# Performance work log

Measured on AMD Instinct MI355X. Metric: run time of the kernel, lower is better.

Reference implementation:

```python
import jax, jax.numpy as jnp
import numpy as np

HM_W, WH_W, OFF_W = 1.0, 0.1, 1.0  # loss_weight dict values
EPS_SIG = 1e-4


def _neg_loss(pred, gt):
    # pred already sigmoided + clamped. Modified focal loss (CornerNet).
    pos = (gt == 1.0).astype(pred.dtype)
    neg = (gt < 1.0).astype(pred.dtype)
    part1 = (pos + (2.0 * neg - 1.0) * pred) ** 2          # alpha=2
    part2 = (neg + (2.0 * pos - 1.0) * gt) ** 4            # beta=4
    part3 = jnp.log(neg + (2.0 * pos - 1.0) * pred)
    loss = -jnp.sum(part1 * part2 * part3)
    num_pos = jnp.sum(pos)
    fallback = jnp.maximum(jnp.sum((pred > 0.3).astype(pred.dtype)), 1.0)
    denom = jnp.where(num_pos == 0.0, fallback, num_pos)
    return loss / denom


def _reg_l1(pred, mask, ind, target):
    # pred: [B,C,H,W] -> gather K per-object C-dim vectors per batch via flat HW index
    B, C, H, W = pred.shape
    K = ind.shape[1]
    feat = pred.transpose(0, 2, 3, 1).reshape(B, H * W, C)  # [B,HW,C]
    idx = jnp.broadcast_to(ind[:, :, None], (B, K, C))
    gathered = jnp.take_along_axis(feat, idx, axis=1)       # [B,K,C]
    m = jnp.broadcast_to(mask[:, :, None].astype(pred.dtype), (B, K, C))
    diff = gathered * m - target * m
    ad = jnp.abs(diff)
    sl1 = jnp.where(ad < 1.0, 0.5 * diff * diff, ad - 0.5)  # smooth_l1, sum
    return jnp.sum(sl1) / (jnp.sum(m) + 1e-4)


def setup_inputs() -> dict:
    key = jax.random.key(0)
    ks = jax.random.split(key, 8)
    B, C, H, W, K = 128, 20, 128, 128, 128
    hm_pred = jax.random.normal(ks[0], (B, C, H, W), dtype=jnp.float32)
    hm_gt = jax.random.uniform(ks[1], (B, C, H, W), dtype=jnp.float32)
    # plant some exact positives (gt == 1) like real CenterNet targets
    hm_gt = hm_gt.at[:, :, 64, 64].set(1.0)
    wh_pred = jax.random.normal(ks[2], (B, 2, H, W), dtype=jnp.float32)
    wh_gt = jax.random.uniform(ks[3], (B, K, 2), dtype=jnp.float32)
    off_pred = jax.random.normal(ks[4], (B, 2, H, W), dtype=jnp.float32)
    off_gt = jax.random.uniform(ks[5], (B, K, 2), dtype=jnp.float32)
    offset_mask = jax.random.randint(ks[6], (B, K), 0, 2, dtype=jnp.int32)
    indexes = jax.random.randint(ks[7], (B, K), 0, H * W).astype(jnp.int64)
    return {"hm_pred": hm_pred, "hm_gt": hm_gt, "wh_pred": wh_pred,
            "wh_gt": wh_gt, "off_pred": off_pred, "off_gt": off_gt,
            "offset_mask": offset_mask, "indexes": indexes}


def reference(hm_pred, hm_gt, wh_pred, wh_gt, off_pred, off_gt, offset_mask, indexes):
    hm = jnp.clip(jax.nn.sigmoid(hm_pred), EPS_SIG, 1.0 - EPS_SIG)
    hm_loss = _neg_loss(hm, hm_gt)
    wh_loss = _reg_l1(wh_pred, offset_mask, indexes, wh_gt)
    off_loss = _reg_l1(off_pred, offset_mask, indexes, off_gt)
    total = HM_W * hm_loss + WH_W * wh_loss + OFF_W * off_loss
    return (hm_loss, wh_loss, off_loss, total)
```

## Files before the change

kernel.cpp:

```cpp
#include <hip/hip_runtime.h>

#define NB_HM   2048
#define NB_REG  64
#define REG_OFF (3 * NB_HM)

typedef float f32x4 __attribute__((ext_vector_type(4)));

__device__ __forceinline__ float wave_sum(float v) {
    #pragma unroll
    for (int off = 32; off > 0; off >>= 1) v += __shfl_down(v, off, 64);
    return v;
}

__device__ __forceinline__ void block_reduce_store3(float a, float b, float c,
                                                    float* __restrict__ dst) {
    a = wave_sum(a); b = wave_sum(b); c = wave_sum(c);
    __shared__ float sa[8], sb[8], sc[8];
    int lane = threadIdx.x & 63;
    int wave = threadIdx.x >> 6;
    if (lane == 0) { sa[wave] = a; sb[wave] = b; sc[wave] = c; }
    __syncthreads();
    if (threadIdx.x == 0) {
        int nw = blockDim.x >> 6;
        float ta = 0.f, tb = 0.f, tc = 0.f;
        for (int w = 0; w < nw; ++w) { ta += sa[w]; tb += sb[w]; tc += sc[w]; }
        dst[0] = ta; dst[1] = tb; dst[2] = tc;
    }
}

__device__ __forceinline__ void hm_elem(float x, float gt, float& s_loss,
                                        unsigned& posc, unsigned& cntc) {
    bool pos = (gt == 1.0f);
    float e = __expf(-x);
    float p = __builtin_amdgcn_rcpf(1.0f + e);
    p = fminf(fmaxf(p, 1e-4f), 1.0f - 1e-4f);
    float arg = pos ? p : 1.0f - p;
    float a   = 1.0f - arg;
    float b   = pos ? 1.0f : 1.0f - gt;
    float b2  = b * b;
    float l   = __logf(arg);
    s_loss += (a * a) * (b2 * b2) * l;
    posc += (unsigned)__popcll(__ballot(pos));
    cntc += (unsigned)__popcll(__ballot(p > 0.3f));
}

#define COMPV(P, G)                                    \
    do {                                               \
        hm_elem((P)[0], (G)[0], s_loss, posc, cntc);   \
        hm_elem((P)[1], (G)[1], s_loss, posc, cntc);   \
        hm_elem((P)[2], (G)[2], s_loss, posc, cntc);   \
        hm_elem((P)[3], (G)[3], s_loss, posc, cntc);   \
    } while (0)

__global__ void __launch_bounds__(256)
hm_loss_kernel(const f32x4* __restrict__ p4,
               const f32x4* __restrict__ g4,
               float* __restrict__ ws, long long N4) {
    float    s_loss = 0.f;
    unsigned posc = 0, cntc = 0;

    if ((N4 % ((long long)NB_HM * 256)) == 0) {
        long long per_block = N4 / NB_HM;
        long long nIter     = per_block >> 8;
        long long i = (long long)blockIdx.x * per_block + threadIdx.x;

        long long j = 0;
        for (; j + 3 < nIter; j += 4, i += 1024) {
            f32x4 xp0 = p4[i];
            f32x4 xp1 = p4[i + 256];
            f32x4 xp2 = p4[i + 512];
            f32x4 xp3 = p4[i + 768];
            f32x4 xg0 = g4[i];
            f32x4 xg1 = g4[i + 256];
            f32x4 xg2 = g4[i + 512];
            f32x4 xg3 = g4[i + 768];
            COMPV(xp0, xg0);
            COMPV(xp1, xg1);
            COMPV(xp2, xg2);
            COMPV(xp3, xg3);
        }
        for (; j < nIter; ++j, i += 256) {
            f32x4 xp = p4[i];
            f32x4 xg = g4[i];
            COMPV(xp, xg);
        }
    } else {
        long long tid = (long long)blockIdx.x * blockDim.x + threadIdx.x;
        long long NT  = (long long)gridDim.x * blockDim.x;
        for (long long i = tid; i < N4; i += NT) {
            f32x4 xp = p4[i];
            f32x4 xg = g4[i];
            COMPV(xp, xg);
        }
    }

    int lane = threadIdx.x & 63;
    float fpos = (lane == 0) ? (float)posc : 0.f;
    float fcnt = (lane == 0) ? (float)cntc : 0.f;
    block_reduce_store3(s_loss, fpos, fcnt, &ws[3 * (size_t)blockIdx.x]);
}

__device__ __forceinline__ float smooth_l1(float d) {
    float ad = fabsf(d);
    return (ad < 1.0f) ? 0.5f * d * d : ad - 0.5f;
}

__global__ void __launch_bounds__(256)
reg_loss_kernel(const float* __restrict__ wh_pred,  const float* __restrict__ wh_gt,
                const float* __restrict__ off_pred, const float* __restrict__ off_gt,
                const int* __restrict__ mask, const int* __restrict__ ind,
                float* __restrict__ ws, int BK, int K, int HW) {
    int t = blockIdx.x * blockDim.x + threadIdx.x;
    int nt = gridDim.x * blockDim.x;
    float s_wh = 0.f, s_off = 0.f, s_m = 0.f;

    for (int i = t; i < BK; i += nt) {
        int b   = i / K;
        float m = (float)mask[i];
        int idx = ind[i];
        const float* wb = wh_pred  + (size_t)b * 2 * HW;
        const float* ob = off_pred + (size_t)b * 2 * HW;
        #pragma unroll
        for (int c = 0; c < 2; ++c) {
            float gw = wb[(size_t)c * HW + idx];
            float tw = wh_gt[(size_t)i * 2 + c];
            s_wh += smooth_l1(gw * m - tw * m);

            float go = ob[(size_t)c * HW + idx];
            float to = off_gt[(size_t)i * 2 + c];
            s_off += smooth_l1(go * m - to * m);
        }
        s_m += 2.0f * m;
    }

    block_reduce_store3(s_wh, s_off, s_m, &ws[REG_OFF + 3 * (size_t)blockIdx.x]);
}

__global__ void __launch_bounds__(1024)
reduce_finalize_kernel(const float* __restrict__ ws, float* __restrict__ out) {
    float a = 0.f, b = 0.f, c = 0.f, w = 0.f, o = 0.f, m = 0.f;
    for (int i = threadIdx.x; i < NB_HM; i += 1024) {
        a += ws[3 * i + 0];
        b += ws[3 * i + 1];
        c += ws[3 * i + 2];
    }
    if (threadIdx.x < 3 * NB_REG) {
        float v = ws[REG_OFF + threadIdx.x];
        int r = threadIdx.x % 3;
        w = (r == 0) ? v : 0.f;
        o = (r == 1) ? v : 0.f;
        m = (r == 2) ? v : 0.f;
    }

    a = wave_sum(a); b = wave_sum(b); c = wave_sum(c);
    w = wave_sum(w); o = wave_sum(o); m = wave_sum(m);

    __shared__ float s[6][16];
    int lane = threadIdx.x & 63, wv = threadIdx.x >> 6;
    if (lane == 0) {
        s[0][wv] = a; s[1][wv] = b; s[2][wv] = c;
        s[3][wv] = w; s[4][wv] = o; s[5][wv] = m;
    }
    __syncthreads();
    if (threadIdx.x == 0) {
        float t[6];
        #pragma unroll
        for (int k = 0; k < 6; ++k) {
            float acc = 0.f;
            for (int q = 0; q < 16; ++q) acc += s[k][q];
            t[k] = acc;
        }
        float loss_sum = -t[0];
        float num_pos  = t[1];
        float fallback = fmaxf(t[2], 1.0f);
        float denom    = (num_pos == 0.0f) ? fallback : num_pos;
        float hm_loss  = loss_sum / denom;
        float md       = t[5] + 1e-4f;
        float wh_loss  = t[3] / md;
        float off_loss = t[4] / md;
        out[0] = hm_loss;
        out[1] = wh_loss;
        out[2] = off_loss;
        out[3] = hm_loss + 0.1f * wh_loss + off_loss;
    }
}

extern "C" void kernel_launch(void* const* d_in, const int* in_sizes, int n_in,
                              void* d_out, int out_size, void* d_ws, size_t ws_size,
                              hipStream_t stream) {
    const float* hm_pred  = (const float*)d_in[0];
    const float* hm_gt    = (const float*)d_in[1];
    const float* wh_pred  = (const float*)d_in[2];
    const float* wh_gt    = (const float*)d_in[3];
    const float* off_pred = (const float*)d_in[4];
    const float* off_gt   = (const float*)d_in[5];
    const int*   mask     = (const int*)d_in[6];
    const int*   ind      = (const int*)d_in[7];
    float*       out      = (float*)d_out;
    float*       ws       = (float*)d_ws;

    long long N  = in_sizes[0];
    int       BK = in_sizes[6];
    const int K  = 128;
    int       B  = BK / K;
    int       HW = in_sizes[2] / (2 * B);

    hm_loss_kernel<<<NB_HM, 256, 0, stream>>>((const f32x4*)hm_pred,
                                              (const f32x4*)hm_gt, ws, N >> 2);
    reg_loss_kernel<<<NB_REG, 256, 0, stream>>>(wh_pred, wh_gt, off_pred, off_gt,
                                                mask, ind, ws, BK, K, HW);
    reduce_finalize_kernel<<<1, 1024, 0, stream>>>(ws, out);
}
```

Baseline: 72.14 us.

## Fuse final reduction into regression kernel via last-block atomic counter; double hm blocks

Removes the separate single-block finalize kernel: the regression kernel's blocks increment an atomic counter, and the last block to finish reads all partial sums and writes the outputs. The counter is reset by the first block of the heatmap kernel, which runs earlier in the same stream. The heatmap grid is doubled to 4096 blocks, so each block handles less data and the final pass reduces more partials. This drops one kernel launch in exchange for a fence and an atomic per regression block.

```diff
diff --git a/kernel.cpp b/kernel.cpp
--- a/kernel.cpp
+++ b/kernel.cpp
@@ -1,8 +1,9 @@
 #include <hip/hip_runtime.h>
 
-#define NB_HM   2048
+#define NB_HM   4096
 #define NB_REG  64
 #define REG_OFF (3 * NB_HM)
+#define CTR_IDX (REG_OFF + 3 * NB_REG)
 
 typedef float f32x4 __attribute__((ext_vector_type(4)));
 
@@ -15,15 +16,15 @@
 __device__ __forceinline__ void block_reduce_store3(float a, float b, float c,
                                                     float* __restrict__ dst) {
     a = wave_sum(a); b = wave_sum(b); c = wave_sum(c);
-    __shared__ float sa[8], sb[8], sc[8];
+    __shared__ float sa[4], sb[4], sc[4];
     int lane = threadIdx.x & 63;
     int wave = threadIdx.x >> 6;
     if (lane == 0) { sa[wave] = a; sb[wave] = b; sc[wave] = c; }
     __syncthreads();
     if (threadIdx.x == 0) {
-        int nw = blockDim.x >> 6;
         float ta = 0.f, tb = 0.f, tc = 0.f;
-        for (int w = 0; w < nw; ++w) { ta += sa[w]; tb += sb[w]; tc += sc[w]; }
+        #pragma unroll
+        for (int w = 0; w < 4; ++w) { ta += sa[w]; tb += sb[w]; tc += sc[w]; }
         dst[0] = ta; dst[1] = tb; dst[2] = tc;
     }
 }
@@ -56,6 +57,9 @@
 hm_loss_kernel(const f32x4* __restrict__ p4,
                const f32x4* __restrict__ g4,
                float* __restrict__ ws, long long N4) {
+    if (blockIdx.x == 0 && threadIdx.x == 0)
+        *(volatile int*)&ws[CTR_IDX] = 0;
+
     float    s_loss = 0.f;
     unsigned posc = 0, cntc = 0;
 
@@ -106,12 +110,13 @@
 }
 
 __global__ void __launch_bounds__(256)
-reg_loss_kernel(const float* __restrict__ wh_pred,  const float* __restrict__ wh_gt,
-                const float* __restrict__ off_pred, const float* __restrict__ off_gt,
-                const int* __restrict__ mask, const int* __restrict__ ind,
-                float* __restrict__ ws, int BK, int K, int HW) {
-    int t = blockIdx.x * blockDim.x + threadIdx.x;
-    int nt = gridDim.x * blockDim.x;
+reg_finalize_kernel(const float* __restrict__ wh_pred,  const float* __restrict__ wh_gt,
+                    const float* __restrict__ off_pred, const float* __restrict__ off_gt,
+                    const int* __restrict__ mask, const int* __restrict__ ind,
+                    float* __restrict__ ws, float* __restrict__ out,
+                    int BK, int K, int HW) {
+    int t  = blockIdx.x * 256 + threadIdx.x;
+    int nt = NB_REG * 256;
     float s_wh = 0.f, s_off = 0.f, s_m = 0.f;
 
     for (int i = t; i < BK; i += nt) {
@@ -134,12 +139,19 @@
     }
 
     block_reduce_store3(s_wh, s_off, s_m, &ws[REG_OFF + 3 * (size_t)blockIdx.x]);
-}
-
-__global__ void __launch_bounds__(1024)
-reduce_finalize_kernel(const float* __restrict__ ws, float* __restrict__ out) {
+
+    __shared__ int s_last;
+    if (threadIdx.x == 0) {
+        __threadfence();
+        int old = atomicAdd((int*)&ws[CTR_IDX], 1);
+        s_last = (old == NB_REG - 1) ? 1 : 0;
+    }
+    __syncthreads();
+    if (!s_last) return;
+    __threadfence();
+
     float a = 0.f, b = 0.f, c = 0.f, w = 0.f, o = 0.f, m = 0.f;
-    for (int i = threadIdx.x; i < NB_HM; i += 1024) {
+    for (int i = threadIdx.x; i < NB_HM; i += 256) {
         a += ws[3 * i + 0];
         b += ws[3 * i + 1];
         c += ws[3 * i + 2];
@@ -155,7 +167,7 @@
     a = wave_sum(a); b = wave_sum(b); c = wave_sum(c);
     w = wave_sum(w); o = wave_sum(o); m = wave_sum(m);
 
-    __shared__ float s[6][16];
+    __shared__ float s[6][4];
     int lane = threadIdx.x & 63, wv = threadIdx.x >> 6;
     if (lane == 0) {
         s[0][wv] = a; s[1][wv] = b; s[2][wv] = c;
@@ -163,21 +175,19 @@
     }
     __syncthreads();
     if (threadIdx.x == 0) {
-        float t[6];
+        float tt[6];
         #pragma unroll
-        for (int k = 0; k < 6; ++k) {
-            float acc = 0.f;
-            for (int q = 0; q < 16; ++q) acc += s[k][q];
-            t[k] = acc;
-        }
-        float loss_sum = -t[0];
-        float num_pos  = t[1];
-        float fallback = fmaxf(t[2], 1.0f);
+        for (int k = 0; k < 6; ++k)
+            tt[k] = s[k][0] + s[k][1] + s[k][2] + s[k][3];
+
+        float loss_sum = -tt[0];
+        float num_pos  = tt[1];
+        float fallback = fmaxf(tt[2], 1.0f);
         float denom    = (num_pos == 0.0f) ? fallback : num_pos;
         float hm_loss  = loss_sum / denom;
-        float md       = t[5] + 1e-4f;
-        float wh_loss  = t[3] / md;
-        float off_loss = t[4] / md;
+        float md       = tt[5] + 1e-4f;
+        float wh_loss  = tt[3] / md;
+        float off_loss = tt[4] / md;
         out[0] = hm_loss;
         out[1] = wh_loss;
         out[2] = off_loss;
@@ -207,7 +217,6 @@
 
     hm_loss_kernel<<<NB_HM, 256, 0, stream>>>((const f32x4*)hm_pred,
                                               (const f32x4*)hm_gt, ws, N >> 2);
-    reg_loss_kernel<<<NB_REG, 256, 0, stream>>>(wh_pred, wh_gt, off_pred, off_gt,
-                                                mask, ind, ws, BK, K, HW);
-    reduce_finalize_kernel<<<1, 1024, 0, stream>>>(ws, out);
-}
+    reg_finalize_kernel<<<NB_REG, 256, 0, stream>>>(wh_pred, wh_gt, off_pred, off_gt,
+                                                    mask, ind, ws, out, BK, K, HW);
+}
```

Result: slower. 73.61 us (+2.0%).
